# Kernel optimization log

Measured on AMD Instinct MI355X. Metric: run time of the kernel, lower is better.

Reference implementation:

```python
import jax, jax.numpy as jnp
import numpy as np

N = 50000          # num_assets / nodes
E = 1_600_000      # edges (avg degree 32)
F = 128            # num_features
R = 4              # num_relations
H = 1              # heads
O1, O2 = 15, 10    # RGATConv out_channels (hard-coded in module)
NEG_SLOPE = 0.2    # leaky_relu slope in RGATConv
BN_EPS = 1e-5


def setup_inputs() -> dict:
    key = jax.random.key(0)
    ks = jax.random.split(key, 24)
    s = 0.1
    return {
        "node_emb": jax.random.normal(ks[0], (N, F), jnp.float32),
        "edge_index": jax.random.randint(ks[1], (2, E), 0, N),
        "edge_types": jax.random.randint(ks[2], (E,), 0, R),
        "edge_attr": jax.random.normal(ks[3], (E, 1), jnp.float32),
        # RGATConv layer 1 params
        "W1": jax.random.normal(ks[4], (R, F, H * O1), jnp.float32) * s,
        "q1": jax.random.normal(ks[5], (H * O1, H), jnp.float32) * s,
        "k1": jax.random.normal(ks[6], (H * O1, H), jnp.float32) * s,
        "e1": jax.random.normal(ks[7], (H * O1, H), jnp.float32) * s,
        "We1": jax.random.normal(ks[8], (1, H * O1), jnp.float32) * s,  # lin_edge
        "b1": jax.random.normal(ks[9], (H * O1,), jnp.float32) * s,
        # RGATConv layer 2 params
        "W2": jax.random.normal(ks[10], (R, H * O1, H * O2), jnp.float32) * s,
        "q2": jax.random.normal(ks[11], (H * O2, H), jnp.float32) * s,
        "k2": jax.random.normal(ks[12], (H * O2, H), jnp.float32) * s,
        "e2": jax.random.normal(ks[13], (H * O2, H), jnp.float32) * s,
        "We2": jax.random.normal(ks[14], (1, H * O2), jnp.float32) * s,
        "b2": jax.random.normal(ks[15], (O2,), jnp.float32) * s,
        # BatchNorm affine params
        "g1": 1.0 + jax.random.normal(ks[16], (H * O1,), jnp.float32) * 0.05,
        "beta1": jax.random.normal(ks[17], (H * O1,), jnp.float32) * 0.05,
        "g2": 1.0 + jax.random.normal(ks[18], (O2,), jnp.float32) * 0.05,
        "beta2": jax.random.normal(ks[19], (O2,), jnp.float32) * 0.05,
        # head Linear(10, 1)
        "w_head": jax.random.normal(ks[20], (O2, 1), jnp.float32) * s,
        "b_head": jax.random.normal(ks[21], (1,), jnp.float32) * s,
    }


def _segment_softmax(alpha, dst, n):
    amax = jax.ops.segment_max(alpha, dst, num_segments=n)
    ex = jnp.exp(alpha - amax[dst])
    denom = jax.ops.segment_sum(ex, dst, num_segments=n)
    return ex / (denom[dst] + 1e-16)


def _rgat(x, src, dst, etype, eattr, W, q, k, e, We, b, heads, out_ch, concat):
    n = x.shape[0]
    # per-relation transform of all nodes, then gather per-edge (same math as
    # PyG's per-edge bmm with W[edge_type])
    xt = jnp.einsum('nf,rfo->nro', x, W)            # [N, R, H*O]
    out_i = xt[dst, etype]                          # [E, H*O] (target)
    out_j = xt[src, etype]                          # [E, H*O] (source)
    alpha = out_i @ q + out_j @ k + (eattr @ We) @ e  # [E, H]
    alpha = jax.nn.leaky_relu(alpha, NEG_SLOPE)
    alpha = _segment_softmax(alpha, dst, n)          # across-relation softmax over dst
    msg = (alpha[:, :, None] * out_j.reshape(-1, heads, out_ch)).reshape(-1, heads * out_ch)
    agg = jax.ops.segment_sum(msg, dst, num_segments=n)
    if not concat:
        agg = agg.reshape(n, heads, out_ch).mean(axis=1)
    return agg + b


def _bn_elu(x, g, beta):
    # training-mode BatchNorm1d (batch statistics, biased variance) + ELU
    mu = x.mean(axis=0)
    var = x.var(axis=0)
    xh = (x - mu) / jnp.sqrt(var + BN_EPS)
    return jax.nn.elu(xh * g + beta)


def reference(node_emb, edge_index, edge_types, edge_attr,
              W1, q1, k1, e1, We1, b1,
              W2, q2, k2, e2, We2, b2,
              g1, beta1, g2, beta2, w_head, b_head):
    src, dst = edge_index[0], edge_index[1]
    x = _rgat(node_emb, src, dst, edge_types, edge_attr,
              W1, q1, k1, e1, We1, b1, H, O1, True)
    x = _bn_elu(x, g1, beta1)
    x = _rgat(x, src, dst, edge_types, edge_attr,
              W2, q2, k2, e2, We2, b2, H, O2, False)
    x = _bn_elu(x, g2, beta2)
    return x @ w_head + b_head                       # [N, 1]
```

## Files before the change

### kernel.cpp

```cpp
#include <hip/hip_runtime.h>


typedef unsigned short ushort_t;
typedef unsigned int uint_t;
typedef __attribute__((ext_vector_type(8))) short bf16x8;
typedef __attribute__((ext_vector_type(4))) float f32x4;

#define NEG_SLOPE 0.2f
#define BN_EPS 1e-5f
#define NBUCK 512

__device__ __forceinline__ float bf2f(ushort_t u) {
    return __uint_as_float(((uint_t)u) << 16);
}
__device__ __forceinline__ ushort_t f2bf(float f) {
    uint_t x = __float_as_uint(f);
    x += 0x7FFFu + ((x >> 16) & 1u);
    return (ushort_t)(x >> 16);
}
__device__ __forceinline__ float loadf(const void* p, int i, int isb) {
    return isb ? bf2f(((const ushort_t*)p)[i]) : ((const float*)p)[i];
}

__global__ __launch_bounds__(256) void k_prep(const uint_t* __restrict__ x,
                                              const void* __restrict__ W1,
                                              const void* __restrict__ W2,
                                              const void* __restrict__ q1b,
                                              const void* __restrict__ k1b,
                                              int* __restrict__ dflag,
                                              int* __restrict__ bcur,
                                              float* __restrict__ stats1,
                                              float* __restrict__ stats2,
                                              ushort_t* __restrict__ Wsw,
                                              float* __restrict__ Wf2, int cap) {
    __shared__ int cnt;
    int t = threadIdx.x;
    if (t == 0) cnt = 0;
    __syncthreads();
    uint_t u = x[t * 37];
    uint_t lo_exp = (u >> 7) & 0xFF;
    atomicAdd(&cnt, (lo_exp >= 96 && lo_exp <= 150) ? 1 : 0);
    __syncthreads();
    int isb = (cnt > 192) ? 1 : 0;
    if (blockIdx.x == 0) {
        if (t == 0) dflag[0] = isb;
        for (int i = t; i < NBUCK; i += 256) bcur[i] = i * cap;
        stats1[t] = 0.f;
        stats2[t] = 0.f;
        for (int idx = t; idx < 15 * 40; idx += 256) {
            int f = idx / 40, j = idx % 40, r = j / 10, o = j % 10;
            Wf2[idx] = loadf(W2, (r * 15 + f) * 10 + o, isb);
        }
    }
    for (int idx = blockIdx.x * 256 + t; idx < 20 * 64 * 8; idx += gridDim.x * 256) {
        int j = idx & 7, lane = (idx >> 3) & 63, fr = idx >> 9;
        int ks = fr / 5, ct = fr % 5;
        int k = ks * 32 + (lane >> 4) * 8 + j;
        int c = ct * 16 + (lane & 15);
        float v = 0.f;
        if (c < 64) {
            int r = c >> 4, o = c & 15;
            if (o < 15) v = loadf(W1, (r * 128 + k) * 15 + o, isb);
        } else if (c < 72) {
            int r = (c - 64) & 3;
            const void* vec = (c < 68) ? q1b : k1b;
            float s = 0.f;
#pragma unroll
            for (int o = 0; o < 15; ++o)
                s += loadf(W1, (r * 128 + k) * 15 + o, isb) * loadf(vec, o, isb);
            v = s;
        }
        Wsw[idx] = f2bf(v);
    }
}

__global__ __launch_bounds__(512) void k_bucket(const int* __restrict__ ei,
                                                const int* __restrict__ et,
                                                const void* __restrict__ ea,
                                                const int* __restrict__ flag,
                                                int* __restrict__ bcur,
                                                int2* __restrict__ tmp,
                                                int E, int npb) {
    extern __shared__ int2 srec[];
    __shared__ int cnt[NBUCK];
    __shared__ int lofs[NBUCK + 1];
    __shared__ int gpos[NBUCK];
    int t = threadIdx.x;
    int isb = flag[0];
    cnt[t] = 0;
    __syncthreads();
    int e0 = blockIdx.x * 8192;
    for (int i = 0; i < 16; ++i) {
        int e = e0 + i * 512 + t;
        if (e < E) atomicAdd(&cnt[ei[E + e] / npb], 1);
    }
    __syncthreads();
    int myc = cnt[t];
    for (int off = 1; off < NBUCK; off <<= 1) {
        int v = (t >= off) ? cnt[t - off] : 0;
        __syncthreads();
        cnt[t] += v;
        __syncthreads();
    }
    lofs[t] = cnt[t] - myc;
    if (t == NBUCK - 1) lofs[NBUCK] = cnt[NBUCK - 1];
    __syncthreads();
    cnt[t] = lofs[t];
    __syncthreads();
    for (int i = 0; i < 16; ++i) {
        int e = e0 + i * 512 + t;
        if (e < E) {
            int d = ei[E + e];
            int b = d / npb;
            int ldst = d - b * npb;
            int idx = atomicAdd(&cnt[b], 1);
            int2 r;
            r.x = (int)((uint_t)ei[e] | ((uint_t)et[e] << 23) | ((uint_t)ldst << 25));
            r.y = __float_as_int(loadf(ea, e, isb));
            srec[idx] = r;
        }
    }
    __syncthreads();
    int c_b = lofs[t + 1] - lofs[t];
    gpos[t] = atomicAdd(&bcur[t], c_b);
    __syncthreads();
    int total = lofs[NBUCK];
    for (int i = t; i < total; i += 512) {
        int lo = 0, hi = NBUCK - 1;
        while (lo < hi) {
            int mid = (lo + hi + 1) >> 1;
            if (lofs[mid] <= i) lo = mid; else hi = mid - 1;
        }
        tmp[gpos[lo] + (i - lofs[lo])] = srec[i];
    }
}

__global__ __launch_bounds__(256) void k_b2csr(const int2* __restrict__ tmp,
                                               const int* __restrict__ bcur,
                                               int* __restrict__ rs,
                                               int* __restrict__ re,
                                               int2* __restrict__ ebuf,
                                               int N, int npb, int cap) {
    __shared__ int cnt[128];
    __shared__ int lofs[129];
    int b = blockIdx.x, t = threadIdx.x;
    int s0 = b * cap;
    int s1 = bcur[b];
    if (t < 128) cnt[t] = 0;
    __syncthreads();
    for (int p = s0 + t; p < s1; p += 256) {
        uint_t x = (uint_t)tmp[p].x;
        atomicAdd(&cnt[(x >> 25) & 0x7F], 1);
    }
    __syncthreads();
    int myc = (t < 128) ? cnt[t] : 0;
    for (int off = 1; off < 128; off <<= 1) {
        int v = (t >= off && t < 128) ? cnt[t - off] : 0;
        __syncthreads();
        if (t < 128) cnt[t] += v;
        __syncthreads();
    }
    if (t < 128) {
        lofs[t] = cnt[t] - myc;
        if (t == 127) lofs[128] = cnt[127];
    }
    __syncthreads();
    int node0 = b * npb;
    if (t < npb && node0 + t < N) {
        rs[node0 + t] = s0 + lofs[t];
        re[node0 + t] = s0 + lofs[t + 1];
    }
    if (t < 128) cnt[t] = lofs[t];
    __syncthreads();
    for (int p = s0 + t; p < s1; p += 256) {
        int2 r = tmp[p];
        uint_t x = (uint_t)r.x;
        int ldst = (x >> 25) & 0x7F;
        int idx = atomicAdd(&cnt[ldst], 1);
        int2 o;
        o.x = (int)(x & 0x7FFFFF) | (((int)(x >> 23) & 3) << 20);
        o.y = (int)(((uint_t)(node0 + ldst) << 16) |
                    (uint_t)f2bf(__int_as_float(r.y)));
        ebuf[s0 + idx] = o;
    }
}

__global__ __launch_bounds__(256) void k_t1(const void* __restrict__ xin,
                                            const ushort_t* __restrict__ Wsw,
                                            const int* __restrict__ flag,
                                            ushort_t* __restrict__ xt,
                                            float* __restrict__ dq,
                                            float* __restrict__ dk,
                                            int N, int ntiles, int nwaves) {
    int isb = flag[0];
    int lane = threadIdx.x & 63;
    int gw = blockIdx.x * 4 + (threadIdx.x >> 6);
    bf16x8 bfr[20];
    const uint4* wq = (const uint4*)Wsw;
#pragma unroll
    for (int fr = 0; fr < 20; ++fr)
        bfr[fr] = __builtin_bit_cast(bf16x8, wq[fr * 64 + lane]);
    int row = lane & 15, quad = lane >> 4;
    for (int tile = gw; tile < ntiles; tile += nwaves) {
        int n0 = tile * 16;
        f32x4 acc[5];
#pragma unroll
        for (int ct = 0; ct < 5; ++ct) acc[ct] = (f32x4){0.f, 0.f, 0.f, 0.f};
        int nA = n0 + row;
        if (nA >= N) nA = N - 1;
#pragma unroll
        for (int ks = 0; ks < 4; ++ks) {
            bf16x8 af;
            if (isb) {
                uint4 u = *(const uint4*)((const ushort_t*)xin + (size_t)nA * 128 + ks * 32 + quad * 8);
                af = __builtin_bit_cast(bf16x8, u);
            } else {
                const float* xf = (const float*)xin + (size_t)nA * 128 + ks * 32 + quad * 8;
#pragma unroll
                for (int j = 0; j < 8; ++j) af[j] = (short)f2bf(xf[j]);
            }
#pragma unroll
            for (int ct = 0; ct < 5; ++ct)
                acc[ct] = __builtin_amdgcn_mfma_f32_16x16x32_bf16(af, bfr[ks * 5 + ct], acc[ct], 0, 0, 0);
        }
#pragma unroll
        for (int i = 0; i < 4; ++i) {
            int n = n0 + quad * 4 + i;
            if (n < N) {
#pragma unroll
                for (int ct = 0; ct < 4; ++ct)
                    xt[(size_t)n * 64 + ct * 16 + row] = f2bf(acc[ct][i]);
                if (row < 4) dq[n * 4 + row] = acc[4][i];
                else if (row < 8) dk[n * 4 + (row - 4)] = acc[4][i];
            }
        }
    }
}

__global__ __launch_bounds__(256) void k_t2(const float* __restrict__ in,
                                            const float* __restrict__ stats,
                                            const void* __restrict__ g,
                                            const void* __restrict__ beta,
                                            const float* __restrict__ Wf,
                                            const void* __restrict__ qb,
                                            const void* __restrict__ kb,
                                            const int* __restrict__ flag,
                                            ushort_t* __restrict__ xt,
                                            float* __restrict__ dq,
                                            float* __restrict__ dk, int N) {
    int isb = flag[0];
    int t = threadIdx.x;
    int lane = t & 63;
    int r = t >> 6;
    int n = blockIdx.x * 64 + lane;
    if (n >= N) return;
    float invN = 1.f / (float)N;
    float v[15];
#pragma unroll
    for (int c = 0; c < 15; ++c) {
        float mean = stats[c * 16] * invN;
        float var = stats[c * 16 + 8] * invN - mean * mean;
        float inv = rsqrtf(var + BN_EPS);
        float h = (in[(size_t)n * 15 + c] - mean) * inv * loadf(g, c, isb) + loadf(beta, c, isb);
        v[c] = h > 0.f ? h : expm1f(h);
    }
    float acc[10];
#pragma unroll
    for (int o = 0; o < 10; ++o) acc[o] = 0.f;
#pragma unroll
    for (int f = 0; f < 15; ++f) {
        const float* wp = Wf + f * 40 + r * 10;
#pragma unroll
        for (int o = 0; o < 10; ++o) acc[o] += v[f] * wp[o];
    }
    float a = 0.f, b = 0.f;
#pragma unroll
    for (int o = 0; o < 10; ++o) {
        a += acc[o] * loadf(qb, o, isb);
        b += acc[o] * loadf(kb, o, isb);
    }
    dq[n * 4 + r] = a;
    dk[n * 4 + r] = b;
    ushort_t* xr = xt + (size_t)n * 64 + r * 16;
    uint_t pk[8];
#pragma unroll
    for (int j = 0; j < 5; ++j)
        pk[j] = (uint_t)f2bf(acc[2 * j]) | ((uint_t)f2bf(acc[2 * j + 1]) << 16);
    pk[5] = 0; pk[6] = 0; pk[7] = 0;
    *(uint4*)(xr)     = make_uint4(pk[0], pk[1], pk[2], pk[3]);
    *(uint4*)(xr + 8) = make_uint4(pk[4], pk[5], pk[6], pk[7]);
}

template <int O>
__global__ __launch_bounds__(256) void k_alpha(const int2* __restrict__ ebuf,
                                               const float* __restrict__ dq,
                                               const float* __restrict__ dk,
                                               const void* __restrict__ Web,
                                               const void* __restrict__ eb,
                                               const int* __restrict__ flag,
                                               int2* __restrict__ ab2, int Etot) {
    int isb = flag[0];
    float c = 0.f;
#pragma unroll
    for (int o = 0; o < O; ++o) c += loadf(Web, o, isb) * loadf(eb, o, isb);
    int e = blockIdx.x * 256 + threadIdx.x;
    if (e >= Etot) return;
    int2 rec = ebuf[e];
    int sr = rec.x & 0xFFFFF, et = rec.x >> 20;
    uint_t y = (uint_t)rec.y;
    int dst = (int)(y >> 16);
    float ea = bf2f((ushort_t)(y & 0xFFFFu));
    float a = dq[dst * 4 + et] + dk[sr * 4 + et] + c * ea;
    a = a > 0.f ? a : NEG_SLOPE * a;
    ab2[e] = make_int2(__float_as_int(__expf(a)), rec.x);
}

template <int O>
__global__ __launch_bounds__(256) void k_gather(const int* __restrict__ rs,
                                                const int* __restrict__ re,
                                                const int2* __restrict__ ab2,
                                                const ushort_t* __restrict__ xt,
                                                const void* __restrict__ bb,
                                                const int* __restrict__ flag,
                                                float* __restrict__ out, int N) {
    int isb = flag[0];
    int lane = threadIdx.x & 63;
    int w = threadIdx.x >> 6;
    int n = blockIdx.x * 4 + w;
    if (n >= N) return;
    int start = rs[n], end = re[n];
    int g = lane >> 4, ch = lane & 15;
    float acc = 0.f, s = 0.f;
    int p = start + g;
    for (; p + 12 < end; p += 16) {
        int2 v0 = ab2[p];
        int2 v1 = ab2[p + 4];
        int2 v2 = ab2[p + 8];
        int2 v3 = ab2[p + 12];
        float x0 = bf2f(xt[(size_t)((v0.y & 0xFFFFF) * 4 + (v0.y >> 20)) * 16 + ch]);
        float x1 = bf2f(xt[(size_t)((v1.y & 0xFFFFF) * 4 + (v1.y >> 20)) * 16 + ch]);
        float x2 = bf2f(xt[(size_t)((v2.y & 0xFFFFF) * 4 + (v2.y >> 20)) * 16 + ch]);
        float x3 = bf2f(xt[(size_t)((v3.y & 0xFFFFF) * 4 + (v3.y >> 20)) * 16 + ch]);
        float e0 = __int_as_float(v0.x), e1 = __int_as_float(v1.x);
        float e2 = __int_as_float(v2.x), e3 = __int_as_float(v3.x);
        s += (e0 + e1) + (e2 + e3);
        acc += e0 * x0;
        acc += e1 * x1;
        acc += e2 * x2;
        acc += e3 * x3;
    }
    for (; p < end; p += 4) {
        int2 v = ab2[p];
        float e = __int_as_float(v.x);
        acc += e * bf2f(xt[(size_t)((v.y & 0xFFFFF) * 4 + (v.y >> 20)) * 16 + ch]);
        s += e;
    }
    s   += __shfl_xor(s, 16, 64);
    s   += __shfl_xor(s, 32, 64);
    acc += __shfl_xor(acc, 16, 64);
    acc += __shfl_xor(acc, 32, 64);
    if (lane < O) out[(size_t)n * O + lane] = acc / (s + 1e-16f) + loadf(bb, lane, isb);
}

template <int C>
__global__ __launch_bounds__(256) void k_bnstats(const float* __restrict__ in,
                                                 float* __restrict__ S, int N) {
    int t = threadIdx.x;
    int ch = t & 15, rg = t >> 4;
    float s1 = 0.f, s2 = 0.f;
    int row0 = blockIdx.x * 256;
    int rowEnd = row0 + 256;
    if (rowEnd > N) rowEnd = N;
    if (ch < C) {
        for (int r = row0 + rg; r < rowEnd; r += 16) {
            float v = in[(size_t)r * C + ch];
            s1 += v;
            s2 += v * v;
        }
    }
    __shared__ float L1[256], L2[256];
    L1[t] = s1; L2[t] = s2;
    __syncthreads();
    for (int k = 128; k >= 16; k >>= 1) {
        if (t < k) { L1[t] += L1[t + k]; L2[t] += L2[t + k]; }
        __syncthreads();
    }
    if (t < C) {
        atomicAdd(&S[t * 16], L1[t]);
        atomicAdd(&S[t * 16 + 8], L2[t]);
    }
}

__global__ __launch_bounds__(256) void k_head(const float* __restrict__ in,
                                              const float* __restrict__ stats,
                                              const void* __restrict__ g,
                                              const void* __restrict__ beta,
                                              const void* __restrict__ wh,
                                              const void* __restrict__ bh,
                                              const int* __restrict__ flag,
                                              void* __restrict__ out, int N) {
    int isb = flag[0];
    int n = blockIdx.x * 256 + threadIdx.x;
    if (n >= N) return;
    float invN = 1.f / (float)N;
    float r = loadf(bh, 0, isb);
#pragma unroll
    for (int c = 0; c < 10; ++c) {
        float mean = stats[c * 16] * invN;
        float var = stats[c * 16 + 8] * invN - mean * mean;
        float inv = rsqrtf(var + BN_EPS);
        float h = (in[(size_t)n * 10 + c] - mean) * inv * loadf(g, c, isb) + loadf(beta, c, isb);
        float e = h > 0.f ? h : expm1f(h);
        r += e * loadf(wh, c, isb);
    }
    if (isb) ((ushort_t*)out)[n] = f2bf(r);
    else     ((float*)out)[n] = r;
}

extern "C" void kernel_launch(void* const* d_in, const int* in_sizes, int n_in,
                              void* d_out, int out_size, void* d_ws, size_t ws_size,
                              hipStream_t stream) {
    const void* node_emb  = d_in[0];
    const int*  edge_index = (const int*)d_in[1];
    const int*  edge_types = (const int*)d_in[2];
    const void* edge_attr = d_in[3];
    const void* W1  = d_in[4];
    const void* q1  = d_in[5];
    const void* k1  = d_in[6];
    const void* e1  = d_in[7];
    const void* We1 = d_in[8];
    const void* b1  = d_in[9];
    const void* W2  = d_in[10];
    const void* q2  = d_in[11];
    const void* k2  = d_in[12];
    const void* e2  = d_in[13];
    const void* We2 = d_in[14];
    const void* b2  = d_in[15];
    const void* g1  = d_in[16];
    const void* beta1 = d_in[17];
    const void* g2  = d_in[18];
    const void* beta2 = d_in[19];
    const void* w_head = d_in[20];
    const void* b_head = d_in[21];

    int N = in_sizes[0] / 128;
    int E = in_sizes[1] / 2;
    int npb = (N + NBUCK - 1) / NBUCK;
    int nbuck = (N + npb - 1) / npb;
    int cap = E / nbuck + 512;
    size_t slots = (size_t)nbuck * cap;

    char* ws = (char*)d_ws;
    size_t off = 0;
    auto alloc = [&](size_t bytes) -> void* {
        void* p = ws + off;
        off = (off + bytes + 255) & ~(size_t)255;
        return p;
    };
    int*   rs      = (int*)alloc((size_t)N * 4);
    int*   re      = (int*)alloc((size_t)N * 4);
    int*   bcur    = (int*)alloc((NBUCK) * 4);
    int*   dflag   = (int*)alloc(256);
    int2*  ebuf    = (int2*)alloc(slots * 8);
    int2*  ab2     = (int2*)alloc(slots * 8);
    size_t big = (size_t)N * 64 * 2;
    if (slots * 8 > big) big = slots * 8;
    ushort_t* xt1  = (ushort_t*)alloc(big);
    int2*  etmp    = (int2*)xt1;
    float* dq1     = (float*)alloc((size_t)N * 16);
    float* dk1     = (float*)alloc((size_t)N * 16);
    float* out1    = (float*)alloc((size_t)N * 15 * 4);
    float* stats1  = (float*)alloc(256 * 4);
    float* stats2  = (float*)alloc(256 * 4);
    ushort_t* Wsw  = (ushort_t*)alloc(20 * 64 * 8 * 2);
    float* Wf2     = (float*)alloc(600 * 4);
    ushort_t* xt2 = xt1;
    float* dq2  = dq1;
    float* dk2  = dk1;
    float* out2 = out1;

    int NB_N = (N + 255) / 256;
    int NB_T2 = (N + 63) / 64;
    int NB_G = (N + 3) / 4;
    int NB_A = (int)((slots + 255) / 256);
    int NB_B = (E + 8191) / 8192;
    int ntiles = (N + 15) / 16;
    int NB_T1 = 391;
    int nwaves = NB_T1 * 4;

    k_prep<<<40, 256, 0, stream>>>((const uint_t*)node_emb, W1, W2, q1, k1,
                                   dflag, bcur, stats1, stats2, Wsw, Wf2, cap);
    k_bucket<<<NB_B, 512, 8192 * sizeof(int2), stream>>>(edge_index, edge_types, edge_attr,
                                                         dflag, bcur, etmp, E, npb);
    k_b2csr<<<nbuck, 256, 0, stream>>>(etmp, bcur, rs, re, ebuf, N, npb, cap);

    k_t1<<<NB_T1, 256, 0, stream>>>(node_emb, Wsw, dflag, xt1, dq1, dk1, N, ntiles, nwaves);
    k_alpha<15><<<NB_A, 256, 0, stream>>>(ebuf, dq1, dk1, We1, e1, dflag, ab2, (int)slots);
    k_gather<15><<<NB_G, 256, 0, stream>>>(rs, re, ab2, xt1, b1, dflag, out1, N);
    k_bnstats<15><<<NB_N, 256, 0, stream>>>(out1, stats1, N);
    k_t2<<<NB_T2, 256, 0, stream>>>(out1, stats1, g1, beta1, Wf2, q2, k2, dflag, xt2, dq2, dk2, N);
    k_alpha<10><<<NB_A, 256, 0, stream>>>(ebuf, dq2, dk2, We2, e2, dflag, ab2, (int)slots);
    k_gather<10><<<NB_G, 256, 0, stream>>>(rs, re, ab2, xt2, b2, dflag, out2, N);
    k_bnstats<10><<<NB_N, 256, 0, stream>>>(out2, stats2, N);
    k_head<<<NB_N, 256, 0, stream>>>(out2, stats2, g2, beta2, w_head, b_head, dflag, d_out, N);
}
```

Baseline: 338.6 us.

## Fuse edge attention into gather and pack key scores into padded feature slot

```diff
diff --git a/kernel.cpp b/kernel.cpp
--- a/kernel.cpp
+++ b/kernel.cpp
@@ -18,8 +18,21 @@
     x += 0x7FFFu + ((x >> 16) & 1u);
     return (ushort_t)(x >> 16);
 }
+__device__ __forceinline__ float h2f(ushort_t u) {
+    _Float16 h = __builtin_bit_cast(_Float16, u);
+    return (float)h;
+}
+__device__ __forceinline__ ushort_t f2h(float f) {
+    _Float16 h = (_Float16)f;
+    return __builtin_bit_cast(ushort_t, h);
+}
 __device__ __forceinline__ float loadf(const void* p, int i, int isb) {
     return isb ? bf2f(((const ushort_t*)p)[i]) : ((const float*)p)[i];
+}
+__device__ __forceinline__ float sel4(float a0, float a1, float a2, float a3, int et) {
+    float lo = (et == 1) ? a1 : a0;
+    float hi = (et == 3) ? a3 : a2;
+    return (et >= 2) ? hi : lo;
 }
 
 __global__ __launch_bounds__(256) void k_prep(const uint_t* __restrict__ x,
@@ -27,10 +40,15 @@
                                               const void* __restrict__ W2,
                                               const void* __restrict__ q1b,
                                               const void* __restrict__ k1b,
+                                              const void* __restrict__ We1,
+                                              const void* __restrict__ e1v,
+                                              const void* __restrict__ We2,
+                                              const void* __restrict__ e2v,
                                               int* __restrict__ dflag,
                                               int* __restrict__ bcur,
                                               float* __restrict__ stats1,
                                               float* __restrict__ stats2,
+                                              float* __restrict__ cbuf,
                                               ushort_t* __restrict__ Wsw,
                                               float* __restrict__ Wf2, int cap) {
     __shared__ int cnt;
@@ -43,7 +61,15 @@
     __syncthreads();
     int isb = (cnt > 192) ? 1 : 0;
     if (blockIdx.x == 0) {
-        if (t == 0) dflag[0] = isb;
+        if (t == 0) {
+            dflag[0] = isb;
+            float c1 = 0.f;
+            for (int o = 0; o < 15; ++o) c1 += loadf(We1, o, isb) * loadf(e1v, o, isb);
+            float c2 = 0.f;
+            for (int o = 0; o < 10; ++o) c2 += loadf(We2, o, isb) * loadf(e2v, o, isb);
+            cbuf[0] = c1;
+            cbuf[1] = c2;
+        }
         for (int i = t; i < NBUCK; i += 256) bcur[i] = i * cap;
         stats1[t] = 0.f;
         stats2[t] = 0.f;
@@ -60,14 +86,21 @@
         float v = 0.f;
         if (c < 64) {
             int r = c >> 4, o = c & 15;
-            if (o < 15) v = loadf(W1, (r * 128 + k) * 15 + o, isb);
-        } else if (c < 72) {
-            int r = (c - 64) & 3;
-            const void* vec = (c < 68) ? q1b : k1b;
+            if (o < 15) {
+                v = loadf(W1, (r * 128 + k) * 15 + o, isb);
+            } else {
+                float s = 0.f;
+#pragma unroll
+                for (int oo = 0; oo < 15; ++oo)
+                    s += loadf(W1, (r * 128 + k) * 15 + oo, isb) * loadf(k1b, oo, isb);
+                v = s;
+            }
+        } else if (c < 68) {
+            int r = c - 64;
             float s = 0.f;
 #pragma unroll
-            for (int o = 0; o < 15; ++o)
-                s += loadf(W1, (r * 128 + k) * 15 + o, isb) * loadf(vec, o, isb);
+            for (int oo = 0; oo < 15; ++oo)
+                s += loadf(W1, (r * 128 + k) * 15 + oo, isb) * loadf(q1b, oo, isb);
             v = s;
         }
         Wsw[idx] = f2bf(v);
@@ -190,7 +223,6 @@
                                             const int* __restrict__ flag,
                                             ushort_t* __restrict__ xt,
                                             float* __restrict__ dq,
-                                            float* __restrict__ dk,
                                             int N, int ntiles, int nwaves) {
     int isb = flag[0];
     int lane = threadIdx.x & 63;
@@ -228,10 +260,12 @@
             int n = n0 + quad * 4 + i;
             if (n < N) {
 #pragma unroll
-                for (int ct = 0; ct < 4; ++ct)
-                    xt[(size_t)n * 64 + ct * 16 + row] = f2bf(acc[ct][i]);
+                for (int ct = 0; ct < 4; ++ct) {
+                    float val = acc[ct][i];
+                    ushort_t bits = (row == 15) ? f2h(val) : f2bf(val);
+                    xt[(size_t)n * 64 + ct * 16 + row] = bits;
+                }
                 if (row < 4) dq[n * 4 + row] = acc[4][i];
-                else if (row < 8) dk[n * 4 + (row - 4)] = acc[4][i];
             }
         }
     }
@@ -246,8 +280,7 @@
                                             const void* __restrict__ kb,
                                             const int* __restrict__ flag,
                                             ushort_t* __restrict__ xt,
-                                            float* __restrict__ dq,
-                                            float* __restrict__ dk, int N) {
+                                            float* __restrict__ dq, int N) {
     int isb = flag[0];
     int t = threadIdx.x;
     int lane = t & 63;
@@ -273,53 +306,31 @@
 #pragma unroll
         for (int o = 0; o < 10; ++o) acc[o] += v[f] * wp[o];
     }
-    float a = 0.f, b = 0.f;
+    float sq = 0.f, sk = 0.f;
 #pragma unroll
     for (int o = 0; o < 10; ++o) {
-        a += acc[o] * loadf(qb, o, isb);
-        b += acc[o] * loadf(kb, o, isb);
-    }
-    dq[n * 4 + r] = a;
-    dk[n * 4 + r] = b;
+        sq += acc[o] * loadf(qb, o, isb);
+        sk += acc[o] * loadf(kb, o, isb);
+    }
+    dq[n * 4 + r] = sq;
     ushort_t* xr = xt + (size_t)n * 64 + r * 16;
     uint_t pk[8];
 #pragma unroll
     for (int j = 0; j < 5; ++j)
         pk[j] = (uint_t)f2bf(acc[2 * j]) | ((uint_t)f2bf(acc[2 * j + 1]) << 16);
-    pk[5] = 0; pk[6] = 0; pk[7] = 0;
+    pk[5] = 0; pk[6] = 0;
+    pk[7] = ((uint_t)f2h(sk)) << 16;
     *(uint4*)(xr)     = make_uint4(pk[0], pk[1], pk[2], pk[3]);
     *(uint4*)(xr + 8) = make_uint4(pk[4], pk[5], pk[6], pk[7]);
-}
-
-template <int O>
-__global__ __launch_bounds__(256) void k_alpha(const int2* __restrict__ ebuf,
-                                               const float* __restrict__ dq,
-                                               const float* __restrict__ dk,
-                                               const void* __restrict__ Web,
-                                               const void* __restrict__ eb,
-                                               const int* __restrict__ flag,
-                                               int2* __restrict__ ab2, int Etot) {
-    int isb = flag[0];
-    float c = 0.f;
-#pragma unroll
-    for (int o = 0; o < O; ++o) c += loadf(Web, o, isb) * loadf(eb, o, isb);
-    int e = blockIdx.x * 256 + threadIdx.x;
-    if (e >= Etot) return;
-    int2 rec = ebuf[e];
-    int sr = rec.x & 0xFFFFF, et = rec.x >> 20;
-    uint_t y = (uint_t)rec.y;
-    int dst = (int)(y >> 16);
-    float ea = bf2f((ushort_t)(y & 0xFFFFu));
-    float a = dq[dst * 4 + et] + dk[sr * 4 + et] + c * ea;
-    a = a > 0.f ? a : NEG_SLOPE * a;
-    ab2[e] = make_int2(__float_as_int(__expf(a)), rec.x);
 }
 
 template <int O>
 __global__ __launch_bounds__(256) void k_gather(const int* __restrict__ rs,
                                                 const int* __restrict__ re,
-                                                const int2* __restrict__ ab2,
+                                                const int2* __restrict__ ebuf,
                                                 const ushort_t* __restrict__ xt,
+                                                const float* __restrict__ dq,
+                                                const float* __restrict__ cp,
                                                 const void* __restrict__ bb,
                                                 const int* __restrict__ flag,
                                                 float* __restrict__ out, int N) {
@@ -329,20 +340,38 @@
     int n = blockIdx.x * 4 + w;
     if (n >= N) return;
     int start = rs[n], end = re[n];
-    int g = lane >> 4, ch = lane & 15;
+    int ch = lane & 15;
+    int gb = lane & 48;
+    bool hi15 = (ch == 15);
+    float c = cp[0];
+    float q0 = dq[n * 4], q1 = dq[n * 4 + 1], q2 = dq[n * 4 + 2], q3 = dq[n * 4 + 3];
     float acc = 0.f, s = 0.f;
-    int p = start + g;
+    int p = start + (gb >> 4);
     for (; p + 12 < end; p += 16) {
-        int2 v0 = ab2[p];
-        int2 v1 = ab2[p + 4];
-        int2 v2 = ab2[p + 8];
-        int2 v3 = ab2[p + 12];
-        float x0 = bf2f(xt[(size_t)((v0.y & 0xFFFFF) * 4 + (v0.y >> 20)) * 16 + ch]);
-        float x1 = bf2f(xt[(size_t)((v1.y & 0xFFFFF) * 4 + (v1.y >> 20)) * 16 + ch]);
-        float x2 = bf2f(xt[(size_t)((v2.y & 0xFFFFF) * 4 + (v2.y >> 20)) * 16 + ch]);
-        float x3 = bf2f(xt[(size_t)((v3.y & 0xFFFFF) * 4 + (v3.y >> 20)) * 16 + ch]);
-        float e0 = __int_as_float(v0.x), e1 = __int_as_float(v1.x);
-        float e2 = __int_as_float(v2.x), e3 = __int_as_float(v3.x);
+        int2 v0 = ebuf[p];
+        int2 v1 = ebuf[p + 4];
+        int2 v2 = ebuf[p + 8];
+        int2 v3 = ebuf[p + 12];
+        ushort_t u0 = xt[(size_t)((v0.x & 0xFFFFF) * 4 + (v0.x >> 20)) * 16 + ch];
+        ushort_t u1 = xt[(size_t)((v1.x & 0xFFFFF) * 4 + (v1.x >> 20)) * 16 + ch];
+        ushort_t u2 = xt[(size_t)((v2.x & 0xFFFFF) * 4 + (v2.x >> 20)) * 16 + ch];
+        ushort_t u3 = xt[(size_t)((v3.x & 0xFFFFF) * 4 + (v3.x >> 20)) * 16 + ch];
+        float x0 = hi15 ? h2f(u0) : bf2f(u0);
+        float x1 = hi15 ? h2f(u1) : bf2f(u1);
+        float x2 = hi15 ? h2f(u2) : bf2f(u2);
+        float x3 = hi15 ? h2f(u3) : bf2f(u3);
+        float dk0 = __shfl(x0, gb + 15, 64);
+        float dk1 = __shfl(x1, gb + 15, 64);
+        float dk2 = __shfl(x2, gb + 15, 64);
+        float dk3 = __shfl(x3, gb + 15, 64);
+        float a0 = sel4(q0, q1, q2, q3, v0.x >> 20) + dk0 + c * bf2f((ushort_t)(v0.y & 0xFFFFu));
+        float a1 = sel4(q0, q1, q2, q3, v1.x >> 20) + dk1 + c * bf2f((ushort_t)(v1.y & 0xFFFFu));
+        float a2 = sel4(q0, q1, q2, q3, v2.x >> 20) + dk2 + c * bf2f((ushort_t)(v2.y & 0xFFFFu));
+        float a3 = sel4(q0, q1, q2, q3, v3.x >> 20) + dk3 + c * bf2f((ushort_t)(v3.y & 0xFFFFu));
+        float e0 = __expf(fmaxf(a0, NEG_SLOPE * a0));
+        float e1 = __expf(fmaxf(a1, NEG_SLOPE * a1));
+        float e2 = __expf(fmaxf(a2, NEG_SLOPE * a2));
+        float e3 = __expf(fmaxf(a3, NEG_SLOPE * a3));
         s += (e0 + e1) + (e2 + e3);
         acc += e0 * x0;
         acc += e1 * x1;
@@ -350,9 +379,13 @@
         acc += e3 * x3;
     }
     for (; p < end; p += 4) {
-        int2 v = ab2[p];
-        float e = __int_as_float(v.x);
-        acc += e * bf2f(xt[(size_t)((v.y & 0xFFFFF) * 4 + (v.y >> 20)) * 16 + ch]);
+        int2 v = ebuf[p];
+        ushort_t u = xt[(size_t)((v.x & 0xFFFFF) * 4 + (v.x >> 20)) * 16 + ch];
+        float x = hi15 ? h2f(u) : bf2f(u);
+        float dk = __shfl(x, gb + 15, 64);
+        float a = sel4(q0, q1, q2, q3, v.x >> 20) + dk + c * bf2f((ushort_t)(v.y & 0xFFFFu));
+        float e = __expf(fmaxf(a, NEG_SLOPE * a));
+        acc += e * x;
         s += e;
     }
     s   += __shfl_xor(s, 16, 64);
@@ -461,14 +494,13 @@
     int*   re      = (int*)alloc((size_t)N * 4);
     int*   bcur    = (int*)alloc((NBUCK) * 4);
     int*   dflag   = (int*)alloc(256);
+    float* cbuf    = (float*)alloc(256);
     int2*  ebuf    = (int2*)alloc(slots * 8);
-    int2*  ab2     = (int2*)alloc(slots * 8);
     size_t big = (size_t)N * 64 * 2;
     if (slots * 8 > big) big = slots * 8;
     ushort_t* xt1  = (ushort_t*)alloc(big);
     int2*  etmp    = (int2*)xt1;
     float* dq1     = (float*)alloc((size_t)N * 16);
-    float* dk1     = (float*)alloc((size_t)N * 16);
     float* out1    = (float*)alloc((size_t)N * 15 * 4);
     float* stats1  = (float*)alloc(256 * 4);
     float* stats2  = (float*)alloc(256 * 4);
@@ -476,31 +508,28 @@
     float* Wf2     = (float*)alloc(600 * 4);
     ushort_t* xt2 = xt1;
     float* dq2  = dq1;
-    float* dk2  = dk1;
     float* out2 = out1;
 
     int NB_N = (N + 255) / 256;
     int NB_T2 = (N + 63) / 64;
     int NB_G = (N + 3) / 4;
-    int NB_A = (int)((slots + 255) / 256);
     int NB_B = (E + 8191) / 8192;
     int ntiles = (N + 15) / 16;
     int NB_T1 = 391;
     int nwaves = NB_T1 * 4;
 
     k_prep<<<40, 256, 0, stream>>>((const uint_t*)node_emb, W1, W2, q1, k1,
-                                   dflag, bcur, stats1, stats2, Wsw, Wf2, cap);
+                                   We1, e1, We2, e2,
+                                   dflag, bcur, stats1, stats2, cbuf, Wsw, Wf2, cap);
     k_bucket<<<NB_B, 512, 8192 * sizeof(int2), stream>>>(edge_index, edge_types, edge_attr,
                                                          dflag, bcur, etmp, E, npb);
     k_b2csr<<<nbuck, 256, 0, stream>>>(etmp, bcur, rs, re, ebuf, N, npb, cap);
 
-    k_t1<<<NB_T1, 256, 0, stream>>>(node_emb, Wsw, dflag, xt1, dq1, dk1, N, ntiles, nwaves);
-    k_alpha<15><<<NB_A, 256, 0, stream>>>(ebuf, dq1, dk1, We1, e1, dflag, ab2, (int)slots);
-    k_gather<15><<<NB_G, 256, 0, stream>>>(rs, re, ab2, xt1, b1, dflag, out1, N);
+    k_t1<<<NB_T1, 256, 0, stream>>>(node_emb, Wsw, dflag, xt1, dq1, N, ntiles, nwaves);
+    k_gather<15><<<NB_G, 256, 0, stream>>>(rs, re, ebuf, xt1, dq1, cbuf, b1, dflag, out1, N);
     k_bnstats<15><<<NB_N, 256, 0, stream>>>(out1, stats1, N);
-    k_t2<<<NB_T2, 256, 0, stream>>>(out1, stats1, g1, beta1, Wf2, q2, k2, dflag, xt2, dq2, dk2, N);
-    k_alpha<10><<<NB_A, 256, 0, stream>>>(ebuf, dq2, dk2, We2, e2, dflag, ab2, (int)slots);
-    k_gather<10><<<NB_G, 256, 0, stream>>>(rs, re, ab2, xt2, b2, dflag, out2, N);
+    k_t2<<<NB_T2, 256, 0, stream>>>(out1, stats1, g1, beta1, Wf2, q2, k2, dflag, xt2, dq2, N);
+    k_gather<10><<<NB_G, 256, 0, stream>>>(rs, re, ebuf, xt2, dq2, cbuf + 1, b2, dflag, out2, N);
     k_bnstats<10><<<NB_N, 256, 0, stream>>>(out2, stats2, N);
     k_head<<<NB_N, 256, 0, stream>>>(out2, stats2, g2, beta2, w_head, b_head, dflag, d_out, N);
 }
```

New measurement: 317.9 us. 1.07x faster.
